# Kernel tuning notes

Hardware: AMD Instinct MI355X
Metric: run time of the kernel (lower is better)

Reference implementation:

```python
import jax, jax.numpy as jnp
import numpy as np

D_MODEL = 192
D_INNER = 384          # expand(2) * d_model
HEADDIM = 12
NHEADS = 32            # d_inner // headdim
DSTATE = 16
NGROUPS = 1
CONV_DIM = D_INNER + 2 * NGROUPS * DSTATE          # 416
D_IN_PROJ = 2 * D_INNER + 2 * NGROUPS * DSTATE + NHEADS  # 832
LN_EPS = 1e-5


def silu(x):
    return x * jax.nn.sigmoid(x)


def depthwise_conv2d(x_nchw, w, b):
    # groups == channels depthwise conv, kernel 3, padding 1 (SAME)
    out = jax.lax.conv_general_dilated(
        x_nchw, w, window_strides=(1, 1), padding='SAME',
        feature_group_count=CONV_DIM,
        dimension_numbers=('NCHW', 'OIHW', 'NCHW'))
    return out + b[None, :, None, None]


def setup_inputs() -> dict:
    key = jax.random.key(0)
    ks = jax.random.split(key, 10)
    Bn, H, W = 4, 128, 128
    u = jax.random.normal(ks[0], (Bn, H, W, D_MODEL), jnp.float32)
    t = jax.random.normal(ks[1], (Bn, H, W, D_MODEL), jnp.float32)
    s_in = 1.0 / np.sqrt(D_MODEL)
    W_in = jax.random.normal(ks[2], (D_IN_PROJ, D_MODEL), jnp.float32) * s_in
    W_t_in = jax.random.normal(ks[3], (D_IN_PROJ, D_MODEL), jnp.float32) * s_in
    conv_w = jax.random.normal(ks[4], (CONV_DIM, 1, 3, 3), jnp.float32) * (1.0 / 3.0)
    conv_b = jnp.zeros((CONV_DIM,), jnp.float32)
    # dt_bias = inverse-softplus of dt sampled log-uniform in [dt_min, dt_max]
    dt0 = jnp.exp(jax.random.uniform(ks[5], (NHEADS,)) * (np.log(0.1) - np.log(0.001)) + np.log(0.001))
    dt_bias = dt0 + jnp.log(-jnp.expm1(-dt0))
    A_log = jnp.log(jax.random.uniform(ks[6], (NHEADS,), minval=1.0, maxval=16.0))
    D = jnp.ones((NHEADS,), jnp.float32)
    ln_gamma = jnp.ones((D_INNER,), jnp.float32)
    ln_beta = jnp.zeros((D_INNER,), jnp.float32)
    W_out = jax.random.normal(ks[7], (D_MODEL, D_INNER), jnp.float32) * (1.0 / np.sqrt(D_INNER))
    return dict(u=u, t=t, W_in=W_in, W_t_in=W_t_in, conv_w=conv_w, conv_b=conv_b,
                dt_bias=dt_bias, A_log=A_log, D=D, ln_gamma=ln_gamma, ln_beta=ln_beta,
                W_out=W_out)


def reference(u, t, W_in, W_t_in, conv_w, conv_b, dt_bias, A_log, D,
              ln_gamma, ln_beta, W_out):
    B0, H, W_, C0 = u.shape
    L = H * W_
    uu = u.reshape(B0, L, C0)
    tt = t.reshape(B0, L, C0)

    # in_proj on main branch: split into z, xBC, dt
    zxbcdt = uu @ W_in.T                                    # (B, L, 832)
    z = zxbcdt[..., :D_INNER]                               # (B, L, 384)
    xBC = zxbcdt[..., D_INNER:D_INNER + CONV_DIM]           # (B, L, 416)
    dt = zxbcdt[..., D_INNER + CONV_DIM:]                   # (B, L, 32)
    dt = jax.nn.softplus(dt + dt_bias)

    # t branch: only x1B1C1 part is ultimately used (C := C1)
    x1B1C1 = (tt @ W_t_in.T)[..., D_INNER:D_INNER + CONV_DIM]

    # depthwise 3x3 conv + silu on both branches
    xBC = xBC.reshape(B0, H, W_, CONV_DIM).transpose(0, 3, 1, 2)
    xBC = silu(depthwise_conv2d(xBC, conv_w, conv_b))
    xBC = xBC.transpose(0, 2, 3, 1).reshape(B0, L, CONV_DIM)

    x1B1C1 = x1B1C1.reshape(B0, H, W_, CONV_DIM).transpose(0, 3, 1, 2)
    x1B1C1 = silu(depthwise_conv2d(x1B1C1, conv_w, conv_b))
    x1B1C1 = x1B1C1.transpose(0, 2, 3, 1).reshape(B0, L, CONV_DIM)

    x = xBC[..., :D_INNER]                                  # V features (B, L, 384)
    Bk = xBC[..., D_INNER:D_INNER + NGROUPS * DSTATE]       # K (B, L, 16)
    Cq = x1B1C1[..., D_INNER + NGROUPS * DSTATE:]           # Q from t-branch (B, L, 16)

    A = -jnp.exp(A_log)                                     # (nheads,), negative

    # non-causal linear attention duality (ngroups == 1)
    V = x.reshape(B0, L, NHEADS, HEADDIM).transpose(0, 2, 1, 3)   # (B, h, L, d)
    dtT = dt.transpose(0, 2, 1)                                   # (B, h, L)
    dA = -(dtT[..., None] * A[None, :, None, None])               # ssd_positve_dA: positive
    V_scaled = V * dA
    KV = jnp.einsum('bln,bhld->bhnd', Bk, V_scaled)               # (B, h, 16, 12)
    y = jnp.einsum('bln,bhnd->bhld', Cq, KV) + V * D[None, :, None, None]
    y = y.transpose(0, 2, 1, 3).reshape(B0, L, D_INNER)

    # LayerNorm over d_inner
    mu = jnp.mean(y, axis=-1, keepdims=True)
    var = jnp.mean((y - mu) ** 2, axis=-1, keepdims=True)
    y = (y - mu) * jax.lax.rsqrt(var + LN_EPS) * ln_gamma + ln_beta

    y = y * z
    out = y @ W_out.T
    return out.reshape(B0, H, W_, C0)
```

## Files before the change

kernel.cpp:

```cpp
#include <hip/hip_runtime.h>
#include <hip/hip_bf16.h>
#include <math.h>


#define BN 4
#define HH 128
#define WWID 128
#define LTOK (HH*WWID)
#define NTOK (BN*LTOK)
#define DMODEL 192
#define DINNER 384
#define NH 32
#define HD 12
#define DST 16
#define CONVD 416
#define KVCHUNKS 64
#define PM 256
#define PBN 64
#define BSTR 200

typedef __hip_bfloat16 bf16;
typedef unsigned int uint32;
typedef unsigned short ushort16;
typedef __attribute__((ext_vector_type(8))) short bf16x8;
typedef __attribute__((ext_vector_type(4))) float f32x4;
typedef __attribute__((ext_vector_type(16))) float f32x16;

__device__ __forceinline__ float bflo(uint32 v){ return __uint_as_float((v & 0xffffu) << 16); }
__device__ __forceinline__ float bfhi(uint32 v){ return __uint_as_float(v & 0xffff0000u); }
__device__ __forceinline__ ushort16 f2bf(float f){
    __hip_bfloat16 h = __float2bfloat16(f);
    return *reinterpret_cast<const ushort16*>(&h);
}
__device__ __forceinline__ float ldbf(const bf16* p){
    return __uint_as_float(((uint32)(*(const ushort16*)p)) << 16);
}
__device__ __forceinline__ float softplusf(float x){
    return (x > 20.f) ? x : log1pf(expf(x));
}
__device__ __forceinline__ float siluf(float x){
    return x / (1.f + expf(-x));
}

union BFPK { short s[8]; bf16x8 v; };

__global__ __launch_bounds__(256) void k_prep(
    const float* __restrict__ Win, const float* __restrict__ Wout,
    const float* __restrict__ cw,
    bf16* __restrict__ Winbf, bf16* __restrict__ Woutbf, float* __restrict__ wtr)
{
    const int i = blockIdx.x*256 + threadIdx.x;
    if (i < 832*DMODEL)   Winbf[i]  = __float2bfloat16(Win[i]);
    if (i < DMODEL*DINNER) Woutbf[i] = __float2bfloat16(Wout[i]);
    if (i < CONVD*9) { const int c = i/9, k = i - c*9; wtr[k*420 + c] = cw[i]; }
}

__global__ __launch_bounds__(512) void k_proj_mfma(
    const float* __restrict__ u, const bf16* __restrict__ Wbf,
    const float* __restrict__ dt_b, const float* __restrict__ A_log,
    bf16* __restrict__ z_bf, bf16* __restrict__ xbc_pre, float* __restrict__ dA)
{
    __shared__ __align__(16) short S[2][PBN*BSTR];

    const int tid = threadIdx.x;
    const int m0 = blockIdx.x * PM;
    const int ntbase  = blockIdx.y * 7;
    const int ntiles  = blockIdx.y ? 6 : 7;
    const int wid = tid >> 6, lane = tid & 63;
    const int fr = lane & 31;
    const int hi = lane >> 5;

    bf16x8 a[12];
    {
        const float* arow = u + (size_t)(m0 + wid*32 + fr)*DMODEL;
        #pragma unroll
        for (int ks=0;ks<12;++ks) {
            const float4 a0 = *(const float4*)(arow + ks*16 + hi*8);
            const float4 a1 = *(const float4*)(arow + ks*16 + hi*8 + 4);
            BFPK pk;
            pk.s[0]=(short)f2bf(a0.x); pk.s[1]=(short)f2bf(a0.y);
            pk.s[2]=(short)f2bf(a0.z); pk.s[3]=(short)f2bf(a0.w);
            pk.s[4]=(short)f2bf(a1.x); pk.s[5]=(short)f2bf(a1.y);
            pk.s[6]=(short)f2bf(a1.z); pk.s[7]=(short)f2bf(a1.w);
            a[ks] = pk.v;
        }
    }

    const int srow = tid >> 3;
    const int sseg = tid & 7;
    uint4 r0, r1, r2;
    auto LOADB = [&](int nt) {
        const short* g = (const short*)Wbf + (size_t)(nt*PBN + srow)*DMODEL + sseg*24;
        r0 = *(const uint4*)g;
        r1 = *(const uint4*)(g + 8);
        r2 = *(const uint4*)(g + 16);
    };
    auto WRITEB = [&](int buf) {
        short* d = &S[buf][srow*BSTR + sseg*24];
        *(uint4*)d        = r0;
        *(uint4*)(d + 8)  = r1;
        *(uint4*)(d + 16) = r2;
    };

    LOADB(ntbase); WRITEB(0);
    LOADB(ntbase + 1);
    __syncthreads();

    for (int i = 0; i < ntiles; ++i) {
        const int nt  = ntbase + i;
        const int cur = i & 1;

        f32x16 acc0, acc1;
        #pragma unroll
        for (int q=0;q<16;++q) { acc0[q]=0.f; acc1[q]=0.f; }

        const short* Sb = &S[cur][0];
        #pragma unroll
        for (int ks=0;ks<12;++ks) {
            const bf16x8 b0 = *(const bf16x8*)&Sb[(fr     )*BSTR + ks*16 + hi*8];
            const bf16x8 b1 = *(const bf16x8*)&Sb[(32 + fr)*BSTR + ks*16 + hi*8];
            acc0 = __builtin_amdgcn_mfma_f32_32x32x16_bf16(a[ks], b0, acc0, 0, 0, 0);
            acc1 = __builtin_amdgcn_mfma_f32_32x32x16_bf16(a[ks], b1, acc1, 0, 0, 0);
        }

        #pragma unroll
        for (int ni=0;ni<2;++ni) {
            const f32x16& ac = ni ? acc1 : acc0;
            const int n0 = nt*64 + ni*32;
            const int n  = n0 + fr;
            if (n0 < DINNER) {
                #pragma unroll
                for (int r=0;r<16;++r) {
                    const int tok = m0 + wid*32 + (r&3) + 8*(r>>2) + 4*hi;
                    z_bf[(size_t)tok*DINNER + n] = __float2bfloat16(ac[r]);
                }
            } else if (n0 < 800) {
                #pragma unroll
                for (int r=0;r<16;++r) {
                    const int tok = m0 + wid*32 + (r&3) + 8*(r>>2) + 4*hi;
                    xbc_pre[(size_t)tok*CONVD + (n - DINNER)] = __float2bfloat16(ac[r]);
                }
            } else {
                const float db = dt_b[fr];
                const float al = expf(A_log[fr]);
                #pragma unroll
                for (int r=0;r<16;++r) {
                    const int tok = m0 + wid*32 + (r&3) + 8*(r>>2) + 4*hi;
                    const float dt = softplusf(ac[r] + db);
                    dA[(size_t)tok*NH + fr] = dt * al;
                }
            }
        }

        if (i + 1 < ntiles) {
            WRITEB(cur ^ 1);
            if (i + 2 < ntiles) LOADB(nt + 2);
        }
        __syncthreads();
    }
}

__global__ __launch_bounds__(256) void k_tproj(
    const float* __restrict__ t, const float* __restrict__ Wtin, float* __restrict__ cq_pre)
{
    __shared__ float ts[16][196];
    __shared__ float ws[16][196];
    const int tid = threadIdx.x;
    const int tok0 = blockIdx.x * 16;
    #pragma unroll
    for (int i = 0; i < 3; ++i) {
        const int flat = tid + 256*i;
        const int row = flat / 48, c = (flat % 48)*4;
        *(float4*)&ts[row][c] = *(const float4*)(t    + (size_t)(tok0+row)*DMODEL + c);
        *(float4*)&ws[row][c] = *(const float4*)(Wtin + (size_t)(784+row)*DMODEL + c);
    }
    __syncthreads();
    const int tt = tid >> 4, n = tid & 15;
    float s0=0.f,s1=0.f,s2=0.f,s3=0.f;
    #pragma unroll 4
    for (int k = 0; k < DMODEL; k += 4) {
        s0 = fmaf(ts[tt][k+0], ws[n][k+0], s0);
        s1 = fmaf(ts[tt][k+1], ws[n][k+1], s1);
        s2 = fmaf(ts[tt][k+2], ws[n][k+2], s2);
        s3 = fmaf(ts[tt][k+3], ws[n][k+3], s3);
    }
    cq_pre[(size_t)(tok0+tt)*DST + n] = (s0+s1)+(s2+s3);
}

__global__ __launch_bounds__(416) void k_conv416(
    const bf16* __restrict__ in, const float* __restrict__ wtr, const float* __restrict__ cb,
    bf16* __restrict__ out)
{
    __shared__ float ws[9*420];
    __shared__ float bs[416];
    const int tid = threadIdx.x;
    for (int i = tid; i < 9*420; i += 416) ws[i] = wtr[i];
    if (tid < 416) bs[tid] = cb[tid];
    __syncthreads();

    const int pl  = tid / 52;
    const int grp = tid - pl*52;
    const int c0  = grp*8;
    const int pix = blockIdx.x*8 + pl;
    const int hw  = pix & (LTOK-1);
    const int h = hw >> 7, w = hw & 127;
    const int bb = pix >> 14;

    float acc[8];
    {
        const float4 b0 = *(const float4*)&bs[c0];
        const float4 b1 = *(const float4*)&bs[c0+4];
        acc[0]=b0.x; acc[1]=b0.y; acc[2]=b0.z; acc[3]=b0.w;
        acc[4]=b1.x; acc[5]=b1.y; acc[6]=b1.z; acc[7]=b1.w;
    }

    #pragma unroll
    for (int dh=-1; dh<=1; ++dh) {
        const int hh = h + dh;
        if ((unsigned)hh >= (unsigned)HH) continue;
        #pragma unroll
        for (int dw=-1; dw<=1; ++dw) {
            const int w2 = w + dw;
            if ((unsigned)w2 >= (unsigned)WWID) continue;
            const int wi = (dh+1)*3 + (dw+1);
            const size_t off = ((size_t)((bb<<14) + (hh<<7) + w2))*CONVD + c0;
            const uint4 v = *(const uint4*)((const ushort16*)in + off);
            const float4 w0 = *(const float4*)&ws[wi*420 + c0];
            const float4 w1 = *(const float4*)&ws[wi*420 + c0 + 4];
            acc[0] = fmaf(bflo(v.x), w0.x, acc[0]);
            acc[1] = fmaf(bfhi(v.x), w0.y, acc[1]);
            acc[2] = fmaf(bflo(v.y), w0.z, acc[2]);
            acc[3] = fmaf(bfhi(v.y), w0.w, acc[3]);
            acc[4] = fmaf(bflo(v.z), w1.x, acc[4]);
            acc[5] = fmaf(bfhi(v.z), w1.y, acc[5]);
            acc[6] = fmaf(bflo(v.w), w1.z, acc[6]);
            acc[7] = fmaf(bfhi(v.w), w1.w, acc[7]);
        }
    }

    uint4 o;
    o.x = ((uint32)f2bf(siluf(acc[1])) << 16) | (uint32)f2bf(siluf(acc[0]));
    o.y = ((uint32)f2bf(siluf(acc[3])) << 16) | (uint32)f2bf(siluf(acc[2]));
    o.z = ((uint32)f2bf(siluf(acc[5])) << 16) | (uint32)f2bf(siluf(acc[4]));
    o.w = ((uint32)f2bf(siluf(acc[7])) << 16) | (uint32)f2bf(siluf(acc[6]));
    *(uint4*)((ushort16*)out + (size_t)pix*CONVD + c0) = o;
}

__global__ __launch_bounds__(256) void k_conv16(
    const float* __restrict__ in, const float* __restrict__ cw, const float* __restrict__ cb,
    bf16* __restrict__ out)
{
    const int idx = blockIdx.x*256 + threadIdx.x;
    const int cc = idx & 15;
    const int pix = idx >> 4;
    const int hw = pix & (LTOK-1);
    const int h = hw >> 7, w = hw & 127;
    const int bb = pix >> 14;
    const int c = 400 + cc;

    float wg[9];
    #pragma unroll
    for (int k=0;k<9;++k) wg[k] = cw[c*9+k];
    float a = cb[c];
    #pragma unroll
    for (int dh=-1; dh<=1; ++dh) {
        const int hh = h + dh;
        if ((unsigned)hh >= (unsigned)HH) continue;
        #pragma unroll
        for (int dw=-1; dw<=1; ++dw) {
            const int w2 = w + dw;
            if ((unsigned)w2 >= (unsigned)WWID) continue;
            a = fmaf(in[((size_t)((bb<<14)+(hh<<7)+w2))*16 + cc], wg[(dh+1)*3 + (dw+1)], a);
        }
    }
    out[(size_t)pix*16 + cc] = __float2bfloat16(siluf(a));
}

__global__ __launch_bounds__(512) void k_kv(
    const bf16* __restrict__ xbc_post, const float* __restrict__ dA,
    float* __restrict__ partial)
{
    __shared__ short vsb[16][408];
    __shared__ float das[16][32];
    const int tid = threadIdx.x;
    const int b = blockIdx.y;
    const int n = tid & 15;
    const int g = tid >> 4;

    float acc[12];
    #pragma unroll
    for (int j=0;j<12;++j) acc[j]=0.f;

    const int l0base = b*LTOK + blockIdx.x*256;

    for (int it = 0; it < 16; ++it) {
        const int l0 = l0base + it*16;
        for (int i = tid; i < 16*200; i += 512) {
            const int tok = i / 200;
            const int c2 = i - tok*200;
            const uint32 v = *(const uint32*)((const ushort16*)xbc_post
                                + (size_t)(l0+tok)*CONVD + c2*2);
            *(uint32*)&vsb[tok][c2*2] = v;
        }
        {
            const int tok = tid >> 5, h = tid & 31;
            das[tok][h] = dA[(size_t)(l0+tok)*NH + h];
        }
        __syncthreads();

        #pragma unroll
        for (int tok = 0; tok < 16; ++tok) {
            const uint32 bkraw = (uint32)(ushort16)vsb[tok][DINNER + n];
            const float s = __uint_as_float(bkraw << 16) * das[tok][g];
            const uint32* vp = (const uint32*)&vsb[tok][g*12];
            const uint32 w0 = vp[0], w1 = vp[1], w2 = vp[2];
            acc[0]  = fmaf(s, bflo(w0), acc[0]);
            acc[1]  = fmaf(s, bfhi(w0), acc[1]);
            acc[2]  = fmaf(s, bflo(w1), acc[2]);
            acc[3]  = fmaf(s, bfhi(w1), acc[3]);
            acc[4]  = fmaf(s, bflo(w2), acc[4]);
            acc[5]  = fmaf(s, bfhi(w2), acc[5]);
            const uint32* vq = (const uint32*)&vsb[tok][g*12 + 6];
            const uint32 w3 = vq[0], w4 = vq[1], w5 = vq[2];
            acc[6]  = fmaf(s, bflo(w3), acc[6]);
            acc[7]  = fmaf(s, bfhi(w3), acc[7]);
            acc[8]  = fmaf(s, bflo(w4), acc[8]);
            acc[9]  = fmaf(s, bfhi(w4), acc[9]);
            acc[10] = fmaf(s, bflo(w5), acc[10]);
            acc[11] = fmaf(s, bfhi(w5), acc[11]);
        }
        __syncthreads();
    }

    float* dst = partial + ((size_t)(b*KVCHUNKS + blockIdx.x))*6144 + (size_t)tid*12;
    #pragma unroll
    for (int j4=0;j4<3;++j4)
        *(float4*)(dst + j4*4) = make_float4(acc[j4*4], acc[j4*4+1], acc[j4*4+2], acc[j4*4+3]);
}

__global__ __launch_bounds__(256) void k_kvred(
    const float* __restrict__ partial, float* __restrict__ kv)
{
    const int idx = blockIdx.x*256 + threadIdx.x;
    const int b = idx / 6144;
    const int flat = idx - b*6144;
    const float* p = partial + (size_t)(b*KVCHUNKS)*6144 + flat;
    float s = 0.f;
    #pragma unroll 4
    for (int c = 0; c < KVCHUNKS; ++c) s += p[(size_t)c*6144];
    kv[idx] = s;
}

__global__ __launch_bounds__(256) void k_ynorm(
    const bf16* __restrict__ xbc_post, const bf16* __restrict__ cq_bf,
    const bf16* __restrict__ z_bf, const float* __restrict__ kv,
    const float* __restrict__ Dv, const float* __restrict__ ln_g, const float* __restrict__ ln_b,
    bf16* __restrict__ yz)
{
    __shared__ __align__(16) short kvb[24*64*8];
    __shared__ float gs[DINNER], bs2[DINNER], ds[DINNER];
    const int tid = threadIdx.x;
    const int token0 = blockIdx.x * 64;
    const int b = token0 >> 14;
    const float* kvB = kv + (size_t)b*6144;

    for (int i = tid; i < DINNER; i += 256) {
        gs[i]  = ln_g[i];
        bs2[i] = ln_b[i];
        ds[i]  = Dv[i/HD];
    }
    #pragma unroll
    for (int it = 0; it < 6; ++it) {
        const int f = tid + 256*it;
        const int t = f >> 6, l = f & 63;
        const int q = l >> 4;
        const int nb = (q & 1)*8;
        const int hd = t*16 + (l & 15);
        const int h = hd/HD, d = hd - h*HD;
        const float* src = kvB + (size_t)h*192 + d;
        BFPK pk;
        #pragma unroll
        for (int i = 0; i < 8; ++i) {
            const float v = src[(size_t)(nb+i)*12];
            if (q < 2) {
                pk.s[i] = (short)f2bf(v);
            } else {
                const uint32 hb = (uint32)(ushort16)f2bf(v);
                pk.s[i] = (short)f2bf(v - __uint_as_float(hb << 16));
            }
        }
        *(bf16x8*)&kvb[(size_t)f*8] = pk.v;
    }
    __syncthreads();

    const int wid = tid >> 6, lane = tid & 63;
    const int fr = lane & 15, fq = lane >> 4;
    const int tokA = token0 + wid*16;

    const bf16x8 cqf = *(const bf16x8*)((const short*)cq_bf + (size_t)(tokA+fr)*DST + (fq&1)*8);

    f32x4 acc[24];
    #pragma unroll
    for (int t = 0; t < 24; ++t) {
        const bf16x8 bfv = *(const bf16x8*)&kvb[(t*64 + lane)*8];
        f32x4 z4 = (f32x4){0.f,0.f,0.f,0.f};
        acc[t] = __builtin_amdgcn_mfma_f32_16x16x32_bf16(cqf, bfv, z4, 0, 0, 0);
    }

    const int tokj0 = tokA + fq*4;
    float s[4]  = {0.f,0.f,0.f,0.f};
    float s2[4] = {0.f,0.f,0.f,0.f};
    #pragma unroll
    for (int t = 0; t < 24; ++t) {
        const int hd = t*16 + fr;
        const float dvh = ds[hd];
        #pragma unroll
        for (int j = 0; j < 4; ++j) {
            const float vv = ldbf(xbc_post + (size_t)(tokj0+j)*CONVD + hd);
            const float y = fmaf(vv, dvh, acc[t][j]);
            acc[t][j] = y;
            s[j] += y;
            s2[j] = fmaf(y, y, s2[j]);
        }
    }
    #pragma unroll
    for (int j = 0; j < 4; ++j) {
        #pragma unroll
        for (int off = 8; off > 0; off >>= 1) {
            s[j]  += __shfl_xor(s[j],  off, 16);
            s2[j] += __shfl_xor(s2[j], off, 16);
        }
    }
    float mu[4], rs[4];
    #pragma unroll
    for (int j = 0; j < 4; ++j) {
        mu[j] = s[j] * (1.f/384.f);
        const float var = s2[j]*(1.f/384.f) - mu[j]*mu[j];
        rs[j] = rsqrtf(var + 1e-5f);
    }

    #pragma unroll
    for (int t = 0; t < 24; ++t) {
        const int hd = t*16 + fr;
        const float g = gs[hd], be = bs2[hd];
        #pragma unroll
        for (int j = 0; j < 4; ++j) {
            const int tok = tokj0 + j;
            const float yn = fmaf((acc[t][j] - mu[j])*rs[j], g, be);
            const float zv = ldbf(z_bf + (size_t)tok*DINNER + hd);
            yz[(size_t)tok*DINNER + hd] = __float2bfloat16(yn*zv);
        }
    }
}

__global__ __launch_bounds__(256) void k_out_mfma(
    const bf16* __restrict__ yz, const bf16* __restrict__ Wbf, float* __restrict__ out)
{
    __shared__ __align__(16) short As[2][128*40];
    __shared__ __align__(16) short Bs[2][192*40];

    const int tid = threadIdx.x;
    const int m0 = blockIdx.x * 128;
    const int wid = tid >> 6, lane = tid & 63;
    const int wm = wid >> 1, wn = wid & 1;
    const int fr = lane & 15, fq = lane >> 4;

    const int arow = tid >> 1, ahalf = tid & 1;
    auto stageA = [&](int ks, int buf) {
        const short* g = (const short*)yz + (size_t)(m0 + arow)*DINNER + ks*32 + ahalf*16;
        const uint4 v0 = *(const uint4*)g;
        const uint4 v1 = *(const uint4*)(g + 8);
        short* d = &As[buf][arow*40 + ahalf*16];
        *(uint4*)d = v0;
        *(uint4*)(d + 8) = v1;
    };
    auto stageB = [&](int ks, int buf) {
        #pragma unroll
        for (int i = 0; i < 3; ++i) {
            const int flat = tid + 256*i;
            const int row = flat >> 2, q = flat & 3;
            const uint4 v = *(const uint4*)((const short*)Wbf + (size_t)row*DINNER + ks*32 + q*8);
            *(uint4*)&Bs[buf][row*40 + q*8] = v;
        }
    };

    f32x4 acc[4][6];
    #pragma unroll
    for (int mi=0;mi<4;++mi)
        #pragma unroll
        for (int ni=0;ni<6;++ni) acc[mi][ni] = (f32x4){0.f,0.f,0.f,0.f};

    stageA(0, 0); stageB(0, 0);
    __syncthreads();

    const int aoff = (wm*64 + fr)*40 + fq*8;
    const int boff = (wn*96 + fr)*40 + fq*8;

    #pragma unroll
    for (int ks = 0; ks < 12; ++ks) {
        const int cur = ks & 1;
        if (ks < 11) { stageA(ks+1, cur^1); stageB(ks+1, cur^1); }
        bf16x8 a[4], b[6];
        #pragma unroll
        for (int mi=0;mi<4;++mi) a[mi] = *(const bf16x8*)(&As[cur][aoff + mi*640]);
        #pragma unroll
        for (int ni=0;ni<6;++ni) b[ni] = *(const bf16x8*)(&Bs[cur][boff + ni*640]);
        #pragma unroll
        for (int mi=0;mi<4;++mi)
            #pragma unroll
            for (int ni=0;ni<6;++ni)
                acc[mi][ni] = __builtin_amdgcn_mfma_f32_16x16x32_bf16(a[mi], b[ni], acc[mi][ni], 0, 0, 0);
        __syncthreads();
    }

    #pragma unroll
    for (int mi=0;mi<4;++mi) {
        #pragma unroll
        for (int j=0;j<4;++j) {
            const int tok = m0 + wm*64 + mi*16 + fq*4 + j;
            #pragma unroll
            for (int ni=0;ni<6;++ni) {
                const int n = wn*96 + ni*16 + fr;
                out[(size_t)tok*DMODEL + n] = acc[mi][ni][j];
            }
        }
    }
}

extern "C" void kernel_launch(void* const* d_in, const int* in_sizes, int n_in,
                              void* d_out, int out_size, void* d_ws, size_t ws_size,
                              hipStream_t stream)
{
    const float* u      = (const float*)d_in[0];
    const float* t      = (const float*)d_in[1];
    const float* Win    = (const float*)d_in[2];
    const float* Wtin   = (const float*)d_in[3];
    const float* conv_w = (const float*)d_in[4];
    const float* conv_b = (const float*)d_in[5];
    const float* dt_b   = (const float*)d_in[6];
    const float* A_log  = (const float*)d_in[7];
    const float* Dv     = (const float*)d_in[8];
    const float* ln_g   = (const float*)d_in[9];
    const float* ln_bt  = (const float*)d_in[10];
    const float* W_out  = (const float*)d_in[11];
    float* out = (float*)d_out;

    char* p = (char*)d_ws;
    bf16* z_bf     = (bf16*)p;  p += (size_t)NTOK*DINNER*2;
    bf16* xbc_pre  = (bf16*)p;  p += (size_t)NTOK*CONVD*2;
    bf16* xbc_post = (bf16*)p;  p += (size_t)NTOK*CONVD*2;
    float* cq_pre  = (float*)p; p += (size_t)NTOK*DST*4;
    bf16* cq_bf    = (bf16*)p;  p += (size_t)NTOK*DST*2;
    float* dA      = (float*)p; p += (size_t)NTOK*NH*4;
    bf16* yz       = (bf16*)p;  p += (size_t)NTOK*DINNER*2;
    float* kv      = (float*)p; p += (size_t)BN*NH*DST*HD*4;
    bf16* Win_bf   = (bf16*)p;  p += (size_t)832*DMODEL*2;
    bf16* Wout_bf  = (bf16*)p;  p += (size_t)DMODEL*DINNER*2;
    float* wtr     = (float*)p; p += (size_t)9*420*4;

    float* kv_part = (float*)xbc_pre;

    k_prep<<<624, 256, 0, stream>>>(Win, W_out, conv_w, Win_bf, Wout_bf, wtr);
    k_proj_mfma<<<dim3(NTOK/PM, 2), 512, 0, stream>>>(u, Win_bf, dt_b, A_log, z_bf, xbc_pre, dA);
    k_tproj<<<NTOK/16, 256, 0, stream>>>(t, Wtin, cq_pre);
    k_conv416<<<NTOK/8, 416, 0, stream>>>(xbc_pre, wtr, conv_b, xbc_post);
    k_conv16<<<NTOK*16/256, 256, 0, stream>>>(cq_pre, conv_w, conv_b, cq_bf);
    k_kv<<<dim3(KVCHUNKS, BN), 512, 0, stream>>>(xbc_post, dA, kv_part);
    k_kvred<<<BN*6144/256, 256, 0, stream>>>(kv_part, kv);
    k_ynorm<<<NTOK/64, 256, 0, stream>>>(xbc_post, cq_bf, z_bf, kv,
                                         Dv, ln_g, ln_bt, yz);
    k_out_mfma<<<512, 256, 0, stream>>>(yz, Wout_bf, out);
}
```

Baseline: 310.9 us.

## Stream W_in tiles via global_load_lds into triple-buffered XOR-swizzled LDS

The in-projection kernel now loads weight tiles straight from global memory into LDS with global_load_lds, using three buffers and explicit vmcnt waits instead of staging through registers. The prep kernel lays out the bf16 weights pre-swizzled (XOR on the k index by row) so LDS reads stay free of bank conflicts without padding. This aims to cut register pressure and VGPR round-trips and to overlap tile loads with MFMA work, at the cost of hand-tuned waitcnt counts that depend on how many stores the compiler emits.

```diff
diff --git a/kernel.cpp b/kernel.cpp
--- a/kernel.cpp
+++ b/kernel.cpp
@@ -16,8 +16,8 @@
 #define CONVD 416
 #define KVCHUNKS 64
 #define PM 256
-#define PBN 64
-#define BSTR 200
+#define TILE_SH 12288
+#define TILE_BY 24576
 
 typedef __hip_bfloat16 bf16;
 typedef unsigned int uint32;
@@ -47,29 +47,49 @@
 __global__ __launch_bounds__(256) void k_prep(
     const float* __restrict__ Win, const float* __restrict__ Wout,
     const float* __restrict__ cw,
-    bf16* __restrict__ Winbf, bf16* __restrict__ Woutbf, float* __restrict__ wtr)
+    bf16* __restrict__ Wsw, bf16* __restrict__ Woutbf, float* __restrict__ wtr)
 {
     const int i = blockIdx.x*256 + threadIdx.x;
-    if (i < 832*DMODEL)   Winbf[i]  = __float2bfloat16(Win[i]);
+    if (i < 832*DMODEL) {
+        const int ch = i / DMODEL, k = i - ch*DMODEL;
+        const int nt = ch >> 6, row = ch & 63;
+        const int ks = k ^ ((row & 7) << 3);
+        Wsw[(size_t)nt*TILE_SH + row*DMODEL + ks] = __float2bfloat16(Win[i]);
+    }
     if (i < DMODEL*DINNER) Woutbf[i] = __float2bfloat16(Wout[i]);
     if (i < CONVD*9) { const int c = i/9, k = i - c*9; wtr[k*420 + c] = cw[i]; }
 }
 
 __global__ __launch_bounds__(512) void k_proj_mfma(
-    const float* __restrict__ u, const bf16* __restrict__ Wbf,
+    const float* __restrict__ u, const bf16* __restrict__ Wsw,
     const float* __restrict__ dt_b, const float* __restrict__ A_log,
     bf16* __restrict__ z_bf, bf16* __restrict__ xbc_pre, float* __restrict__ dA)
 {
-    __shared__ __align__(16) short S[2][PBN*BSTR];
+    __shared__ __align__(16) short S[3*TILE_SH];
 
     const int tid = threadIdx.x;
     const int m0 = blockIdx.x * PM;
-    const int ntbase  = blockIdx.y * 7;
-    const int ntiles  = blockIdx.y ? 6 : 7;
+    const int ntbase = blockIdx.y * 7;
+    const int ntiles = blockIdx.y ? 6 : 7;
     const int wid = tid >> 6, lane = tid & 63;
     const int fr = lane & 31;
     const int hi = lane >> 5;
 
+    const char* gW = (const char*)Wsw;
+    auto GLOAD = [&](int nt, int buf) {
+        const char* src = gW + (size_t)nt*TILE_BY + wid*3072 + lane*16;
+        char* dst = ((char*)S) + buf*TILE_BY + wid*3072;
+        #pragma unroll
+        for (int c = 0; c < 3; ++c)
+            __builtin_amdgcn_global_load_lds(
+                (const __attribute__((address_space(1))) void*)(src + c*1024),
+                (__attribute__((address_space(3))) void*)(dst + c*1024), 16, 0, 0);
+    };
+
+    GLOAD(ntbase, 0);
+
+    const float db = dt_b[fr];
+    const float al = expf(A_log[fr]);
     bf16x8 a[12];
     {
         const float* arow = u + (size_t)(m0 + wid*32 + fr)*DMODEL;
@@ -85,40 +105,26 @@
             a[ks] = pk.v;
         }
     }
-
-    const int srow = tid >> 3;
-    const int sseg = tid & 7;
-    uint4 r0, r1, r2;
-    auto LOADB = [&](int nt) {
-        const short* g = (const short*)Wbf + (size_t)(nt*PBN + srow)*DMODEL + sseg*24;
-        r0 = *(const uint4*)g;
-        r1 = *(const uint4*)(g + 8);
-        r2 = *(const uint4*)(g + 16);
-    };
-    auto WRITEB = [&](int buf) {
-        short* d = &S[buf][srow*BSTR + sseg*24];
-        *(uint4*)d        = r0;
-        *(uint4*)(d + 8)  = r1;
-        *(uint4*)(d + 16) = r2;
-    };
-
-    LOADB(ntbase); WRITEB(0);
-    LOADB(ntbase + 1);
-    __syncthreads();
+    asm volatile("s_waitcnt vmcnt(0)" ::: "memory");
+    GLOAD(ntbase + 1, 1);
+    __builtin_amdgcn_s_barrier();
+    __builtin_amdgcn_sched_barrier(0);
+
+    const int kswz = (fr & 7) << 3;
 
     for (int i = 0; i < ntiles; ++i) {
-        const int nt  = ntbase + i;
-        const int cur = i & 1;
+        const int nt = ntbase + i;
+        const short* Sb = &S[(i % 3)*TILE_SH];
 
         f32x16 acc0, acc1;
         #pragma unroll
         for (int q=0;q<16;++q) { acc0[q]=0.f; acc1[q]=0.f; }
 
-        const short* Sb = &S[cur][0];
         #pragma unroll
         for (int ks=0;ks<12;++ks) {
-            const bf16x8 b0 = *(const bf16x8*)&Sb[(fr     )*BSTR + ks*16 + hi*8];
-            const bf16x8 b1 = *(const bf16x8*)&Sb[(32 + fr)*BSTR + ks*16 + hi*8];
+            const int kk = (ks*16 + hi*8) ^ kswz;
+            const bf16x8 b0 = *(const bf16x8*)&Sb[fr*DMODEL + kk];
+            const bf16x8 b1 = *(const bf16x8*)&Sb[(32+fr)*DMODEL + kk];
             acc0 = __builtin_amdgcn_mfma_f32_32x32x16_bf16(a[ks], b0, acc0, 0, 0, 0);
             acc1 = __builtin_amdgcn_mfma_f32_32x32x16_bf16(a[ks], b1, acc1, 0, 0, 0);
         }
@@ -141,8 +147,6 @@
                     xbc_pre[(size_t)tok*CONVD + (n - DINNER)] = __float2bfloat16(ac[r]);
                 }
             } else {
-                const float db = dt_b[fr];
-                const float al = expf(A_log[fr]);
                 #pragma unroll
                 for (int r=0;r<16;++r) {
                     const int tok = m0 + wid*32 + (r&3) + 8*(r>>2) + 4*hi;
@@ -152,11 +156,14 @@
             }
         }
 
-        if (i + 1 < ntiles) {
-            WRITEB(cur ^ 1);
-            if (i + 2 < ntiles) LOADB(nt + 2);
-        }
-        __syncthreads();
+        if (i + 2 < ntiles) {
+            GLOAD(nt + 2, (i + 2) % 3);
+            asm volatile("s_waitcnt vmcnt(35)" ::: "memory");
+        } else {
+            asm volatile("s_waitcnt vmcnt(32)" ::: "memory");
+        }
+        __builtin_amdgcn_s_barrier();
+        __builtin_amdgcn_sched_barrier(0);
     }
 }
 
@@ -554,14 +561,14 @@
     float* dA      = (float*)p; p += (size_t)NTOK*NH*4;
     bf16* yz       = (bf16*)p;  p += (size_t)NTOK*DINNER*2;
     float* kv      = (float*)p; p += (size_t)BN*NH*DST*HD*4;
-    bf16* Win_bf   = (bf16*)p;  p += (size_t)832*DMODEL*2;
+    bf16* Wsw      = (bf16*)p;  p += (size_t)832*DMODEL*2;
     bf16* Wout_bf  = (bf16*)p;  p += (size_t)DMODEL*DINNER*2;
     float* wtr     = (float*)p; p += (size_t)9*420*4;
 
     float* kv_part = (float*)xbc_pre;
 
-    k_prep<<<624, 256, 0, stream>>>(Win, W_out, conv_w, Win_bf, Wout_bf, wtr);
-    k_proj_mfma<<<dim3(NTOK/PM, 2), 512, 0, stream>>>(u, Win_bf, dt_b, A_log, z_bf, xbc_pre, dA);
+    k_prep<<<624, 256, 0, stream>>>(Win, W_out, conv_w, Wsw, Wout_bf, wtr);
+    k_proj_mfma<<<dim3(NTOK/PM, 2), 512, 0, stream>>>(u, Wsw, dt_b, A_log, z_bf, xbc_pre, dA);
     k_tproj<<<NTOK/16, 256, 0, stream>>>(t, Wtin, cq_pre);
     k_conv416<<<NTOK/8, 416, 0, stream>>>(xbc_pre, wtr, conv_b, xbc_post);
     k_conv16<<<NTOK*16/256, 256, 0, stream>>>(cq_pre, conv_w, conv_b, cq_bf);
```

Result: no change. 311.2 us (+0.1%).
